# Kernel tuning notes

Measured on AMD Instinct MI355X. Metric: run time of the kernel, lower is better.

## Reference

```python
import jax, jax.numpy as jnp
import numpy as np

B, H, W, C = 32, 32, 32, 512
HEADS, WS, SS = 16, 8, 4
N = WS * WS            # tokens per window
NW = (H // WS) * (W // WS)  # windows per image
HD = C // HEADS
EPS = 1e-5


def _np_window_partition(x, ws):
    b, h, w, c = x.shape
    x = x.reshape(b, h // ws, ws, w // ws, ws, c).transpose(0, 1, 3, 2, 4, 5)
    return x.reshape(-1, ws, ws, c)


def _make_attn_mask():
    img = np.zeros((1, H, W, 1), np.float32)
    sl = (slice(0, -WS), slice(-WS, -SS), slice(-SS, None))
    cnt = 0
    for hs in sl:
        for ws_ in sl:
            img[:, hs, ws_, :] = cnt
            cnt += 1
    mw = _np_window_partition(img, WS).reshape(-1, N)
    d = mw[:, None, :] - mw[:, :, None]
    return np.where(d != 0, np.float32(-100.0), np.float32(0.0))  # [nW, N, N]


def _rel_pos_index():
    coords = np.stack(np.meshgrid(np.arange(WS), np.arange(WS), indexing='ij'))  # [2,ws,ws]
    cf = coords.reshape(2, -1)
    rel = cf[:, :, None] - cf[:, None, :]          # [2,N,N]
    rel = rel.transpose(1, 2, 0)                    # [N,N,2]
    rel[:, :, 0] += WS - 1
    rel[:, :, 1] += WS - 1
    rel[:, :, 0] *= 2 * WS - 1
    return rel.sum(-1)                              # [N,N]

_ATTN_MASK = jnp.asarray(_make_attn_mask())
_RPI = jnp.asarray(_rel_pos_index())


def _ln(x, w, b):
    mu = jnp.mean(x, -1, keepdims=True)
    var = jnp.mean(jnp.square(x - mu), -1, keepdims=True)
    return (x - mu) * jax.lax.rsqrt(var + EPS) * w + b


def _modulate(x, shift, scale):
    return x * (1.0 + scale[:, None, :]) + shift[:, None, :]


def setup_inputs() -> dict:
    key = jax.random.key(0)
    ks = jax.random.split(key, 8)
    s = lambda fan: 1.0 / np.sqrt(fan)
    return {
        'x': jax.random.normal(ks[0], (B, H * W, C), jnp.float32),
        'cond': jax.random.normal(ks[1], (B, C), jnp.float32),
        'norm1_w': jnp.ones((C,), jnp.float32),
        'norm1_b': jnp.zeros((C,), jnp.float32),
        'qkv_w': jax.random.normal(ks[2], (3 * C, C), jnp.float32) * s(C),
        'qkv_b': jnp.zeros((3 * C,), jnp.float32),
        'rpb_table': jax.random.normal(ks[3], ((2 * WS - 1) ** 2, HEADS), jnp.float32) * 0.02,
        'proj_w': jax.random.normal(ks[4], (C, C), jnp.float32) * s(C),
        'proj_b': jnp.zeros((C,), jnp.float32),
        'norm2_w': jnp.ones((C,), jnp.float32),
        'norm2_b': jnp.zeros((C,), jnp.float32),
        'fc1_w': jax.random.normal(ks[5], (4 * C, C), jnp.float32) * s(C),
        'fc1_b': jnp.zeros((4 * C,), jnp.float32),
        'fc2_w': jax.random.normal(ks[6], (C, 4 * C), jnp.float32) * s(4 * C),
        'fc2_b': jnp.zeros((C,), jnp.float32),
        'ada_w': jax.random.normal(ks[7], (6 * C, C), jnp.float32) * s(C),
        'ada_b': jnp.zeros((6 * C,), jnp.float32),
    }


def reference(x, cond, norm1_w, norm1_b, qkv_w, qkv_b, rpb_table, proj_w, proj_b,
              norm2_w, norm2_b, fc1_w, fc1_b, fc2_w, fc2_b, ada_w, ada_b):
    # adaLN modulation params
    ada = jax.nn.silu(cond) @ ada_w.T + ada_b                      # [B, 6C]
    sh_msa, sc_msa, g_msa, sh_mlp, sc_mlp, g_mlp = jnp.split(ada, 6, axis=1)

    shortcut = x
    h = _modulate(_ln(x, norm1_w, norm1_b), sh_msa, sc_msa)        # [B, L, C]
    h = h.reshape(B, H, W, C)
    h = jnp.roll(h, shift=(-SS, -SS), axis=(1, 2))                 # cyclic shift

    # window partition -> [B*nW, N, C]
    hw = h.reshape(B, H // WS, WS, W // WS, WS, C).transpose(0, 1, 3, 2, 4, 5)
    hw = hw.reshape(B * NW, N, C)

    # window attention with relative position bias + shift mask
    qkv = (hw @ qkv_w.T + qkv_b).reshape(B * NW, N, 3, HEADS, HD)
    qkv = qkv.transpose(2, 0, 3, 1, 4)                             # [3, B_, heads, N, hd]
    q, k, v = qkv[0], qkv[1], qkv[2]
    attn = jnp.einsum('bhnd,bhmd->bhnm', q * (HD ** -0.5), k)      # [B_, heads, N, N]
    rpb = rpb_table[_RPI.reshape(-1)].reshape(N, N, HEADS).transpose(2, 0, 1)
    attn = attn + rpb[None]
    attn = attn.reshape(B, NW, HEADS, N, N) + _ATTN_MASK[None, :, None]
    attn = jax.nn.softmax(attn.reshape(B * NW, HEADS, N, N), axis=-1)
    out = jnp.einsum('bhnm,bhmd->bhnd', attn, v)                   # [B_, heads, N, hd]
    out = out.transpose(0, 2, 1, 3).reshape(B * NW, N, C)
    out = out @ proj_w.T + proj_b

    # window reverse -> [B, H, W, C]
    out = out.reshape(B, H // WS, W // WS, WS, WS, C).transpose(0, 1, 3, 2, 4, 5)
    out = out.reshape(B, H, W, C)
    out = jnp.roll(out, shift=(SS, SS), axis=(1, 2)).reshape(B, H * W, C)

    x = shortcut + g_msa[:, None, :] * out

    m = _modulate(_ln(x, norm2_w, norm2_b), sh_mlp, sc_mlp)
    m = jax.nn.gelu(m @ fc1_w.T + fc1_b, approximate=False) @ fc2_w.T + fc2_b
    return x + g_mlp[:, None, :] * m
```

## Files before the change

### kernel.cpp

```cpp
#include <hip/hip_runtime.h>
#include <math.h>

typedef unsigned short u16;
typedef short short8 __attribute__((ext_vector_type(8)));
typedef float floatx4 __attribute__((ext_vector_type(4)));

#define SS 4
#define C_DIM 512
#define L_TOK 1024

static __device__ __forceinline__ u16 f2bf(float f) {
  union { float f; unsigned u; } v; v.f = f;
  unsigned u = v.u;
  unsigned r = (u + 0x7fffu + ((u >> 16) & 1u)) >> 16;
  return (u16)r;
}

typedef const __attribute__((address_space(1))) void* gvp;
typedef __attribute__((address_space(3))) void* lvp;
#define ASYNC16(g, l) __builtin_amdgcn_global_load_lds((gvp)(g), (lvp)(l), 16, 0, 0)

__global__ __launch_bounds__(256) void convert_bf16(const float* __restrict__ src,
                                                    u16* __restrict__ dst, int n4) {
  int i = blockIdx.x * 256 + threadIdx.x;
  if (i >= n4) return;
  float4 v = ((const float4*)src)[i];
  ushort4 o;
  o.x = f2bf(v.x); o.y = f2bf(v.y); o.z = f2bf(v.z); o.w = f2bf(v.w);
  ((ushort4*)dst)[i] = o;
}

__global__ __launch_bounds__(256) void ada_kernel(const float* __restrict__ cond,
                                                  const float* __restrict__ w,
                                                  const float* __restrict__ bias,
                                                  float* __restrict__ ada) {
  int b = blockIdx.y;
  int j = blockIdx.x * 256 + threadIdx.x;
  __shared__ float sc[C_DIM];
  for (int c = threadIdx.x; c < C_DIM; c += 256) {
    float v = cond[b * C_DIM + c];
    sc[c] = v / (1.0f + expf(-v));
  }
  __syncthreads();
  const float* wr = w + (size_t)j * C_DIM;
  float acc = 0.f;
  for (int k = 0; k < C_DIM; k += 4) {
    float4 wv = *(const float4*)&wr[k];
    acc += sc[k] * wv.x + sc[k + 1] * wv.y + sc[k + 2] * wv.z + sc[k + 3] * wv.w;
  }
  ada[(size_t)b * 3072 + j] = acc + bias[j];
}

__global__ __launch_bounds__(64) void prep_attn(const float* __restrict__ rpb,
                                                float* __restrict__ rpbT,
                                                unsigned long long* __restrict__ maskbits) {
  int q = blockIdx.x;
  int head = blockIdx.y;
  int k = threadIdx.x;
  int i1 = q >> 3, j1 = q & 7, i2 = k >> 3, j2 = k & 7;
  rpbT[((size_t)head * 64 + q) * 64 + k] =
      rpb[((i1 - i2 + 7) * 15 + (j1 - j2 + 7)) * 16 + head];
  if (head == 0) {
    for (int widx = 0; widx < 16; widx++) {
      int wh = widx >> 2, wwi = widx & 3;
      int iq = q >> 3, jq = q & 7, ik = k >> 3, jk = k & 7;
      int hq = wh * 8 + iq, wq = wwi * 8 + jq;
      int hk = wh * 8 + ik, wk = wwi * 8 + jk;
      int rq = ((hq < 24) ? 0 : (hq < 28) ? 1 : 2) * 3 + ((wq < 24) ? 0 : (wq < 28) ? 1 : 2);
      int rk = ((hk < 24) ? 0 : (hk < 28) ? 1 : 2) * 3 + ((wk < 24) ? 0 : (wk < 28) ? 1 : 2);
      unsigned long long m = __ballot(rq != rk);
      if (k == 0) maskbits[widx * 64 + q] = m;
    }
  }
}

template <int MODE>
__global__ __launch_bounds__(128) void ln_mod(const float* __restrict__ x,
                                              const float* __restrict__ ada,
                                              const float* __restrict__ nw,
                                              const float* __restrict__ nb,
                                              u16* __restrict__ out) {
  int m = blockIdx.x;
  int b = m >> 10;
  size_t srow;
  if (MODE == 0) {
    int n = m & 63, widx = (m >> 6) & 15;
    int wh = widx >> 2, wwi = widx & 3;
    int i = n >> 3, j = n & 7;
    int hs = (wh * 8 + i + SS) & 31;
    int ws_ = (wwi * 8 + j + SS) & 31;
    srow = (size_t)b * L_TOK + hs * 32 + ws_;
  } else {
    srow = (size_t)m;
  }
  const float* src = x + srow * C_DIM;
  int t = threadIdx.x;
  float4 v = *(const float4*)&src[t * 4];
  float s = v.x + v.y + v.z + v.w;
  float ss = v.x * v.x + v.y * v.y + v.z * v.z + v.w * v.w;
#pragma unroll
  for (int off = 32; off > 0; off >>= 1) {
    s += __shfl_down(s, off);
    ss += __shfl_down(ss, off);
  }
  __shared__ float red[4];
  if ((t & 63) == 0) { red[(t >> 6) * 2] = s; red[(t >> 6) * 2 + 1] = ss; }
  __syncthreads();
  float mean = (red[0] + red[2]) * (1.f / C_DIM);
  float var = (red[1] + red[3]) * (1.f / C_DIM) - mean * mean;
  float rstd = rsqrtf(var + 1e-5f);
  const float* sh = ada + (size_t)b * 3072 + (MODE ? 1536 : 0);
  const float* scm = ada + (size_t)b * 3072 + (MODE ? 2048 : 512);
  int c = t * 4;
  ushort4 o;
  {
    float y;
    y = ((v.x - mean) * rstd * nw[c + 0] + nb[c + 0]) * (1.f + scm[c + 0]) + sh[c + 0]; o.x = f2bf(y);
    y = ((v.y - mean) * rstd * nw[c + 1] + nb[c + 1]) * (1.f + scm[c + 1]) + sh[c + 1]; o.y = f2bf(y);
    y = ((v.z - mean) * rstd * nw[c + 2] + nb[c + 2]) * (1.f + scm[c + 2]) + sh[c + 2]; o.z = f2bf(y);
    y = ((v.w - mean) * rstd * nw[c + 3] + nb[c + 3]) * (1.f + scm[c + 3]) + sh[c + 3]; o.w = f2bf(y);
  }
  *(ushort4*)&out[(size_t)m * C_DIM + c] = o;
}

template <int EPI>
__global__ __launch_bounds__(256, 2) void gemm_bf16(
    const u16* __restrict__ A, const u16* __restrict__ Bw,
    const float* __restrict__ bias, int K, int N,
    u16* __restrict__ outBf, float* __restrict__ outF,
    const float* __restrict__ resid, const float* __restrict__ ada) {
  __shared__ __align__(16) u16 lA[128 * 32];
  __shared__ __align__(16) u16 lB[128 * 32];
  const int tid = threadIdx.x;
  const int lane = tid & 63, wave = tid >> 6;
  const int wr = wave >> 1, wc = wave & 1;
  const int rowA0 = blockIdx.y * 128;
  const int colB0 = blockIdx.x * 128;
  floatx4 acc[4][4];
#pragma unroll
  for (int a = 0; a < 4; a++)
#pragma unroll
    for (int b = 0; b < 4; b++) acc[a][b] = (floatx4){0.f, 0.f, 0.f, 0.f};

  const int r0 = tid >> 2, c0 = (tid & 3) * 8;
  const int r1 = r0 + 64;
  const int q = lane >> 4, fr = lane & 15;

  const u16* gA0 = &A[(size_t)(rowA0 + r0) * K + c0];
  const u16* gA1 = &A[(size_t)(rowA0 + r1) * K + c0];
  const u16* gB0 = &Bw[(size_t)(colB0 + r0) * K + c0];
  const u16* gB1 = &Bw[(size_t)(colB0 + r1) * K + c0];
  u16* lA0 = &lA[wave * 512];
  u16* lA1 = &lA[2048 + wave * 512];
  u16* lB0 = &lB[wave * 512];
  u16* lB1 = &lB[2048 + wave * 512];

  for (int k0 = 0; k0 < K; k0 += 32) {
    ASYNC16(gA0 + k0, lA0);
    ASYNC16(gA1 + k0, lA1);
    ASYNC16(gB0 + k0, lB0);
    ASYNC16(gB1 + k0, lB1);
    __syncthreads();
    short8 af[4], bfr[4];
#pragma unroll
    for (int mi = 0; mi < 4; mi++)
      af[mi] = *(const short8*)&lA[(wr * 64 + mi * 16 + fr) * 32 + q * 8];
#pragma unroll
    for (int ni = 0; ni < 4; ni++)
      bfr[ni] = *(const short8*)&lB[(wc * 64 + ni * 16 + fr) * 32 + q * 8];
#pragma unroll
    for (int mi = 0; mi < 4; mi++)
#pragma unroll
      for (int ni = 0; ni < 4; ni++)
        acc[mi][ni] = __builtin_amdgcn_mfma_f32_16x16x32_bf16(af[mi], bfr[ni], acc[mi][ni], 0, 0, 0);
    __syncthreads();
  }

#pragma unroll
  for (int mi = 0; mi < 4; mi++) {
#pragma unroll
    for (int ni = 0; ni < 4; ni++) {
      int col = colB0 + wc * 64 + ni * 16 + fr;
      float bv = bias[col];
#pragma unroll
      for (int r = 0; r < 4; r++) {
        int row = rowA0 + wr * 64 + mi * 16 + q * 4 + r;
        float v = acc[mi][ni][r] + bv;
        if (EPI == 0) {
          outBf[(size_t)row * N + col] = f2bf(v);
        } else if (EPI == 1) {
          v = 0.5f * v * (1.f + erff(v * 0.70710678118654752f));
          outBf[(size_t)row * N + col] = f2bf(v);
        } else if (EPI == 2) {
          int b = row >> 10;
          int n = row & 63, widx = (row >> 6) & 15;
          int wh = widx >> 2, wwi = widx & 3;
          int i = n >> 3, j = n & 7;
          int hd = (wh * 8 + i + SS) & 31;
          int wd = (wwi * 8 + j + SS) & 31;
          size_t dst = ((size_t)b * L_TOK + hd * 32 + wd) * C_DIM + col;
          outF[dst] = resid[dst] + ada[(size_t)b * 3072 + 1024 + col] * v;
        } else {
          int b = row >> 10;
          size_t dst = (size_t)row * C_DIM + col;
          outF[dst] = outF[dst] + ada[(size_t)b * 3072 + 2560 + col] * v;
        }
      }
    }
  }
}

__global__ __launch_bounds__(256, 2) void attn_mfma(const u16* __restrict__ qkv,
                                                    const float* __restrict__ rpbT,
                                                    const unsigned long long* __restrict__ maskbits,
                                                    u16* __restrict__ out) {
  __shared__ __align__(16) u16 sVT[4][32 * 72];
  __shared__ __align__(16) u16 sP[4][64 * 72];
  const int tid = threadIdx.x, wave = tid >> 6, lane = tid & 63;
  const int col = lane & 15, quad = lane >> 4;
  const int id = blockIdx.x * 4 + wave;
  const int w_ = id >> 4, head = id & 15;
  const int widx = w_ & 15;
  u16* VT = sVT[wave];
  u16* P = sP[wave];
  const u16* base = qkv + (size_t)w_ * 64 * 1536 + head * 32;

  {
    const u16* vrow = base + 1024 + (size_t)lane * 1536;
#pragma unroll
    for (int c = 0; c < 4; c++) {
      uint4 u = *(const uint4*)&vrow[c * 8];
      unsigned uu0 = u.x, uu1 = u.y, uu2 = u.z, uu3 = u.w;
      VT[(c * 8 + 0) * 72 + lane] = (u16)(uu0 & 0xffff);
      VT[(c * 8 + 1) * 72 + lane] = (u16)(uu0 >> 16);
      VT[(c * 8 + 2) * 72 + lane] = (u16)(uu1 & 0xffff);
      VT[(c * 8 + 3) * 72 + lane] = (u16)(uu1 >> 16);
      VT[(c * 8 + 4) * 72 + lane] = (u16)(uu2 & 0xffff);
      VT[(c * 8 + 5) * 72 + lane] = (u16)(uu2 >> 16);
      VT[(c * 8 + 6) * 72 + lane] = (u16)(uu3 & 0xffff);
      VT[(c * 8 + 7) * 72 + lane] = (u16)(uu3 >> 16);
    }
  }

  short8 kf[4], qf[4];
#pragma unroll
  for (int mi = 0; mi < 4; mi++)
    kf[mi] = *(const short8*)(base + 512 + (size_t)(mi * 16 + col) * 1536 + quad * 8);
#pragma unroll
  for (int ni = 0; ni < 4; ni++)
    qf[ni] = *(const short8*)(base + (size_t)(ni * 16 + col) * 1536 + quad * 8);

  floatx4 st[4][4];
#pragma unroll
  for (int mi = 0; mi < 4; mi++)
#pragma unroll
    for (int ni = 0; ni < 4; ni++) st[mi][ni] = (floatx4){0.f, 0.f, 0.f, 0.f};
#pragma unroll
  for (int mi = 0; mi < 4; mi++)
#pragma unroll
    for (int ni = 0; ni < 4; ni++)
      st[mi][ni] = __builtin_amdgcn_mfma_f32_16x16x32_bf16(kf[mi], qf[ni], st[mi][ni], 0, 0, 0);

  const float scale = 0.17677669529663687f;
  float invq[4];
#pragma unroll
  for (int ni = 0; ni < 4; ni++) {
    int q = ni * 16 + col;
    unsigned long long mw = maskbits[widx * 64 + q];
    const float* rp = rpbT + ((size_t)head * 64 + q) * 64;
    float mx = -1e30f;
#pragma unroll
    for (int mi = 0; mi < 4; mi++) {
      floatx4 r4 = *(const floatx4*)&rp[mi * 16 + quad * 4];
#pragma unroll
      for (int r = 0; r < 4; r++) {
        int key = mi * 16 + quad * 4 + r;
        float s = st[mi][ni][r] * scale + r4[r];
        s -= ((mw >> key) & 1ull) ? 100.f : 0.f;
        st[mi][ni][r] = s;
        mx = fmaxf(mx, s);
      }
    }
    mx = fmaxf(mx, __shfl_xor(mx, 16));
    mx = fmaxf(mx, __shfl_xor(mx, 32));
    float sum = 0.f;
#pragma unroll
    for (int mi = 0; mi < 4; mi++) {
      float e0 = __expf(st[mi][ni][0] - mx);
      float e1 = __expf(st[mi][ni][1] - mx);
      float e2 = __expf(st[mi][ni][2] - mx);
      float e3 = __expf(st[mi][ni][3] - mx);
      sum += e0 + e1 + e2 + e3;
      ushort4 pk;
      pk.x = f2bf(e0); pk.y = f2bf(e1); pk.z = f2bf(e2); pk.w = f2bf(e3);
      *(ushort4*)&P[q * 72 + mi * 16 + quad * 4] = pk;
    }
    sum += __shfl_xor(sum, 16);
    sum += __shfl_xor(sum, 32);
    invq[ni] = 1.f / sum;
  }

  floatx4 o[2][4];
#pragma unroll
  for (int mt = 0; mt < 2; mt++)
#pragma unroll
    for (int nt = 0; nt < 4; nt++) o[mt][nt] = (floatx4){0.f, 0.f, 0.f, 0.f};
#pragma unroll
  for (int kc = 0; kc < 2; kc++) {
    short8 vf0 = *(const short8*)&VT[(col) * 72 + kc * 32 + quad * 8];
    short8 vf1 = *(const short8*)&VT[(16 + col) * 72 + kc * 32 + quad * 8];
#pragma unroll
    for (int nt = 0; nt < 4; nt++) {
      short8 pf = *(const short8*)&P[(nt * 16 + col) * 72 + kc * 32 + quad * 8];
      o[0][nt] = __builtin_amdgcn_mfma_f32_16x16x32_bf16(vf0, pf, o[0][nt], 0, 0, 0);
      o[1][nt] = __builtin_amdgcn_mfma_f32_16x16x32_bf16(vf1, pf, o[1][nt], 0, 0, 0);
    }
  }

#pragma unroll
  for (int mt = 0; mt < 2; mt++)
#pragma unroll
    for (int nt = 0; nt < 4; nt++) {
      int q = nt * 16 + col;
      float iv = invq[nt];
      ushort4 pk;
      pk.x = f2bf(o[mt][nt][0] * iv);
      pk.y = f2bf(o[mt][nt][1] * iv);
      pk.z = f2bf(o[mt][nt][2] * iv);
      pk.w = f2bf(o[mt][nt][3] * iv);
      *(ushort4*)&out[((size_t)w_ * 64 + q) * 512 + head * 32 + mt * 16 + quad * 4] = pk;
    }
}

extern "C" void kernel_launch(void* const* d_in, const int* in_sizes, int n_in,
                              void* d_out, int out_size, void* d_ws, size_t ws_size,
                              hipStream_t stream) {
  const float* x      = (const float*)d_in[0];
  const float* cond   = (const float*)d_in[1];
  const float* n1w    = (const float*)d_in[2];
  const float* n1b    = (const float*)d_in[3];
  const float* qkv_w  = (const float*)d_in[4];
  const float* qkv_b  = (const float*)d_in[5];
  const float* rpb    = (const float*)d_in[6];
  const float* proj_w = (const float*)d_in[7];
  const float* proj_b = (const float*)d_in[8];
  const float* n2w    = (const float*)d_in[9];
  const float* n2b    = (const float*)d_in[10];
  const float* fc1_w  = (const float*)d_in[11];
  const float* fc1_b  = (const float*)d_in[12];
  const float* fc2_w  = (const float*)d_in[13];
  const float* fc2_b  = (const float*)d_in[14];
  const float* ada_w  = (const float*)d_in[15];
  const float* ada_b  = (const float*)d_in[16];
  float* out = (float*)d_out;
  char* ws = (char*)d_ws;

  u16*  qkvw_bf  = (u16*)(ws + 0);
  u16*  projw_bf = (u16*)(ws + 1572864);
  u16*  fc1w_bf  = (u16*)(ws + 2097152);
  u16*  fc2w_bf  = (u16*)(ws + 4194304);
  float* ada     = (float*)(ws + 6291456);
  float* rpbT    = (float*)(ws + 6684672);
  unsigned long long* maskb = (unsigned long long*)(ws + 6946816);
  u16*  hw       = (u16*)(ws + 6955008);
  u16*  qkvo     = (u16*)(ws + 40509440);
  u16*  attno    = (u16*)(ws + 141172736);
  u16*  mlp      = (u16*)(ws + 40509440);

  convert_bf16<<<768, 256, 0, stream>>>(qkv_w, qkvw_bf, 196608);
  convert_bf16<<<256, 256, 0, stream>>>(proj_w, projw_bf, 65536);
  convert_bf16<<<1024, 256, 0, stream>>>(fc1_w, fc1w_bf, 262144);
  convert_bf16<<<1024, 256, 0, stream>>>(fc2_w, fc2w_bf, 262144);
  prep_attn<<<dim3(64, 16), 64, 0, stream>>>(rpb, rpbT, maskb);

  ada_kernel<<<dim3(12, 32), 256, 0, stream>>>(cond, ada_w, ada_b, ada);
  ln_mod<0><<<32768, 128, 0, stream>>>(x, ada, n1w, n1b, hw);
  gemm_bf16<0><<<dim3(12, 256), 256, 0, stream>>>(hw, qkvw_bf, qkv_b, 512, 1536,
                                                  qkvo, nullptr, nullptr, nullptr);
  attn_mfma<<<2048, 256, 0, stream>>>(qkvo, rpbT, maskb, attno);
  gemm_bf16<2><<<dim3(4, 256), 256, 0, stream>>>(attno, projw_bf, proj_b, 512, 512,
                                                 nullptr, out, x, ada);
  ln_mod<1><<<32768, 128, 0, stream>>>(out, ada, n2w, n2b, hw);
  gemm_bf16<1><<<dim3(16, 256), 256, 0, stream>>>(hw, fc1w_bf, fc1_b, 512, 2048,
                                                  mlp, nullptr, nullptr, nullptr);
  gemm_bf16<3><<<dim3(4, 256), 256, 0, stream>>>(mlp, fc2w_bf, fc2_b, 2048, 512,
                                                 nullptr, out, nullptr, ada);
}
```

Measured before the change: 618.0 us.

## Widen GEMM K-step to 64, transpose MFMA operands for vectorized epilogue, approximate GELU

The GEMM now loads 64-wide K slices per barrier pair, splitting them into two LDS halves, which halves the number of synchronisations. It also swaps the MFMA operand order so each lane holds four consecutive output columns. That lets the epilogue use float4 bias, residual and ada loads and packed stores instead of scalar strided stores. The exact erf GELU is replaced with a sigmoid-based tanh approximation, which trades accuracy for cheaper math. LDS use doubles, which may affect occupancy.

```diff
diff --git a/kernel.cpp b/kernel.cpp
--- a/kernel.cpp
+++ b/kernel.cpp
@@ -63,9 +63,8 @@
   if (head == 0) {
     for (int widx = 0; widx < 16; widx++) {
       int wh = widx >> 2, wwi = widx & 3;
-      int iq = q >> 3, jq = q & 7, ik = k >> 3, jk = k & 7;
-      int hq = wh * 8 + iq, wq = wwi * 8 + jq;
-      int hk = wh * 8 + ik, wk = wwi * 8 + jk;
+      int hq = wh * 8 + i1, wq = wwi * 8 + j1;
+      int hk = wh * 8 + i2, wk = wwi * 8 + j2;
       int rq = ((hq < 24) ? 0 : (hq < 28) ? 1 : 2) * 3 + ((wq < 24) ? 0 : (wq < 28) ? 1 : 2);
       int rk = ((hk < 24) ? 0 : (hk < 28) ? 1 : 2) * 3 + ((wk < 24) ? 0 : (wk < 28) ? 1 : 2);
       unsigned long long m = __ballot(rq != rk);
@@ -129,8 +128,8 @@
     const float* __restrict__ bias, int K, int N,
     u16* __restrict__ outBf, float* __restrict__ outF,
     const float* __restrict__ resid, const float* __restrict__ ada) {
-  __shared__ __align__(16) u16 lA[128 * 32];
-  __shared__ __align__(16) u16 lB[128 * 32];
+  __shared__ __align__(16) u16 lA[2][128 * 32];
+  __shared__ __align__(16) u16 lB[2][128 * 32];
   const int tid = threadIdx.x;
   const int lane = tid & 63, wave = tid >> 6;
   const int wr = wave >> 1, wc = wave & 1;
@@ -143,68 +142,86 @@
     for (int b = 0; b < 4; b++) acc[a][b] = (floatx4){0.f, 0.f, 0.f, 0.f};
 
   const int r0 = tid >> 2, c0 = (tid & 3) * 8;
-  const int r1 = r0 + 64;
   const int q = lane >> 4, fr = lane & 15;
 
-  const u16* gA0 = &A[(size_t)(rowA0 + r0) * K + c0];
-  const u16* gA1 = &A[(size_t)(rowA0 + r1) * K + c0];
-  const u16* gB0 = &Bw[(size_t)(colB0 + r0) * K + c0];
-  const u16* gB1 = &Bw[(size_t)(colB0 + r1) * K + c0];
-  u16* lA0 = &lA[wave * 512];
-  u16* lA1 = &lA[2048 + wave * 512];
-  u16* lB0 = &lB[wave * 512];
-  u16* lB1 = &lB[2048 + wave * 512];
-
-  for (int k0 = 0; k0 < K; k0 += 32) {
-    ASYNC16(gA0 + k0, lA0);
-    ASYNC16(gA1 + k0, lA1);
-    ASYNC16(gB0 + k0, lB0);
-    ASYNC16(gB1 + k0, lB1);
+  const u16* gA = &A[(size_t)(rowA0 + r0) * K + c0];
+  const u16* gB = &Bw[(size_t)(colB0 + r0) * K + c0];
+  const size_t up = (size_t)64 * K;
+  u16* lA0 = &lA[0][wave * 512];
+  u16* lB0 = &lB[0][wave * 512];
+
+  for (int k0 = 0; k0 < K; k0 += 64) {
+    ASYNC16(gA + k0, lA0);
+    ASYNC16(gA + k0 + up, lA0 + 2048);
+    ASYNC16(gA + k0 + 32, lA0 + 4096);
+    ASYNC16(gA + k0 + 32 + up, lA0 + 6144);
+    ASYNC16(gB + k0, lB0);
+    ASYNC16(gB + k0 + up, lB0 + 2048);
+    ASYNC16(gB + k0 + 32, lB0 + 4096);
+    ASYNC16(gB + k0 + 32 + up, lB0 + 6144);
     __syncthreads();
-    short8 af[4], bfr[4];
-#pragma unroll
-    for (int mi = 0; mi < 4; mi++)
-      af[mi] = *(const short8*)&lA[(wr * 64 + mi * 16 + fr) * 32 + q * 8];
-#pragma unroll
-    for (int ni = 0; ni < 4; ni++)
-      bfr[ni] = *(const short8*)&lB[(wc * 64 + ni * 16 + fr) * 32 + q * 8];
-#pragma unroll
-    for (int mi = 0; mi < 4; mi++)
+#pragma unroll
+    for (int kc = 0; kc < 2; kc++) {
+      short8 xf[4], wf[4];
+#pragma unroll
+      for (int mi = 0; mi < 4; mi++)
+        xf[mi] = *(const short8*)&lA[kc][(wr * 64 + mi * 16 + fr) * 32 + q * 8];
 #pragma unroll
       for (int ni = 0; ni < 4; ni++)
-        acc[mi][ni] = __builtin_amdgcn_mfma_f32_16x16x32_bf16(af[mi], bfr[ni], acc[mi][ni], 0, 0, 0);
+        wf[ni] = *(const short8*)&lB[kc][(wc * 64 + ni * 16 + fr) * 32 + q * 8];
+#pragma unroll
+      for (int mi = 0; mi < 4; mi++)
+#pragma unroll
+        for (int ni = 0; ni < 4; ni++)
+          acc[mi][ni] = __builtin_amdgcn_mfma_f32_16x16x32_bf16(wf[ni], xf[mi], acc[mi][ni], 0, 0, 0);
+    }
     __syncthreads();
   }
 
 #pragma unroll
   for (int mi = 0; mi < 4; mi++) {
+    int row = rowA0 + wr * 64 + mi * 16 + fr;
 #pragma unroll
     for (int ni = 0; ni < 4; ni++) {
-      int col = colB0 + wc * 64 + ni * 16 + fr;
-      float bv = bias[col];
-#pragma unroll
-      for (int r = 0; r < 4; r++) {
-        int row = rowA0 + wr * 64 + mi * 16 + q * 4 + r;
-        float v = acc[mi][ni][r] + bv;
-        if (EPI == 0) {
-          outBf[(size_t)row * N + col] = f2bf(v);
-        } else if (EPI == 1) {
-          v = 0.5f * v * (1.f + erff(v * 0.70710678118654752f));
-          outBf[(size_t)row * N + col] = f2bf(v);
-        } else if (EPI == 2) {
-          int b = row >> 10;
-          int n = row & 63, widx = (row >> 6) & 15;
-          int wh = widx >> 2, wwi = widx & 3;
-          int i = n >> 3, j = n & 7;
-          int hd = (wh * 8 + i + SS) & 31;
-          int wd = (wwi * 8 + j + SS) & 31;
-          size_t dst = ((size_t)b * L_TOK + hd * 32 + wd) * C_DIM + col;
-          outF[dst] = resid[dst] + ada[(size_t)b * 3072 + 1024 + col] * v;
-        } else {
-          int b = row >> 10;
-          size_t dst = (size_t)row * C_DIM + col;
-          outF[dst] = outF[dst] + ada[(size_t)b * 3072 + 2560 + col] * v;
-        }
+      int col0 = colB0 + wc * 64 + ni * 16 + q * 4;
+      float4 bv = *(const float4*)&bias[col0];
+      float v0 = acc[mi][ni][0] + bv.x;
+      float v1 = acc[mi][ni][1] + bv.y;
+      float v2 = acc[mi][ni][2] + bv.z;
+      float v3 = acc[mi][ni][3] + bv.w;
+      if (EPI == 1) {
+        v0 = __fdividef(v0, 1.f + __expf(-v0 * (1.59576912f + 0.07135481f * v0 * v0)));
+        v1 = __fdividef(v1, 1.f + __expf(-v1 * (1.59576912f + 0.07135481f * v1 * v1)));
+        v2 = __fdividef(v2, 1.f + __expf(-v2 * (1.59576912f + 0.07135481f * v2 * v2)));
+        v3 = __fdividef(v3, 1.f + __expf(-v3 * (1.59576912f + 0.07135481f * v3 * v3)));
+      }
+      if (EPI == 0 || EPI == 1) {
+        ushort4 pk;
+        pk.x = f2bf(v0); pk.y = f2bf(v1); pk.z = f2bf(v2); pk.w = f2bf(v3);
+        *(ushort4*)&outBf[(size_t)row * N + col0] = pk;
+      } else if (EPI == 2) {
+        int b = row >> 10;
+        int n = row & 63, widx = (row >> 6) & 15;
+        int wh = widx >> 2, wwi = widx & 3;
+        int i = n >> 3, j = n & 7;
+        int hd = (wh * 8 + i + SS) & 31;
+        int wd = (wwi * 8 + j + SS) & 31;
+        size_t dst = ((size_t)b * L_TOK + hd * 32 + wd) * C_DIM + col0;
+        float4 rs = *(const float4*)&resid[dst];
+        float4 g = *(const float4*)&ada[(size_t)b * 3072 + 1024 + col0];
+        float4 o;
+        o.x = rs.x + g.x * v0; o.y = rs.y + g.y * v1;
+        o.z = rs.z + g.z * v2; o.w = rs.w + g.w * v3;
+        *(float4*)&outF[dst] = o;
+      } else {
+        int b = row >> 10;
+        size_t dst = (size_t)row * C_DIM + col0;
+        float4 cur = *(const float4*)&outF[dst];
+        float4 g = *(const float4*)&ada[(size_t)b * 3072 + 2560 + col0];
+        float4 o;
+        o.x = cur.x + g.x * v0; o.y = cur.y + g.y * v1;
+        o.z = cur.z + g.z * v2; o.w = cur.w + g.w * v3;
+        *(float4*)&outF[dst] = o;
       }
     }
   }
```

After: 592.8 us. 4.1% less time.
